# Kernel optimization log

Measured on AMD Instinct MI355X. Metric: run time of the kernel, lower is better.

Reference implementation:

```python
import jax, jax.numpy as jnp
import numpy as np

N_NODES = 50000
N_EDGES = 800000
IN_DIM = 128
OUT_DIM = 64
NEG_SLOPE = 0.2
EPS = 1e-8


def setup_inputs() -> dict:
    key = jax.random.key(0)
    k1, k2, k3, k4, k5 = jax.random.split(key, 5)
    x = jax.random.normal(k1, (N_NODES, IN_DIM), dtype=jnp.float32)
    edge_index = jax.random.randint(k2, (2, N_EDGES), 0, N_NODES, dtype=jnp.int64)
    # xavier-like scale for the linear weight
    W = jax.random.normal(k3, (IN_DIM, OUT_DIM), dtype=jnp.float32) * (1.0 / np.sqrt(IN_DIM))
    att_src = jax.random.normal(k4, (OUT_DIM,), dtype=jnp.float32) * 0.1
    att_dst = jax.random.normal(k5, (OUT_DIM,), dtype=jnp.float32) * 0.1
    bias = jnp.zeros((OUT_DIM,), dtype=jnp.float32)
    return {"x": x, "edge_index": edge_index, "W": W,
            "att_src": att_src, "att_dst": att_dst, "bias": bias}


def reference(x, edge_index, W, att_src, att_dst, bias):
    src, dst = edge_index[0], edge_index[1]
    h = x @ W                                  # (N, F_out)
    h_src = h[src]                             # (E, F_out) gather
    # per-edge score: a_src^T h_i + a_dst^T h_j
    e = h_src @ att_src + h[dst] @ att_dst     # (E,)
    e = jax.nn.leaky_relu(e, NEG_SLOPE)
    alpha = jax.nn.sigmoid(e)
    # per-dst normalization (sigmoid attention, not softmax)
    denom = jax.ops.segment_sum(alpha, dst, num_segments=N_NODES) + EPS  # (N,)
    alpha = alpha / denom[dst]
    msg = h_src * alpha[:, None]               # (E, F_out)
    out = jax.ops.segment_sum(msg, dst, num_segments=N_NODES)  # (N, F_out)
    return out + bias
```

## Files before the change

kernel.cpp:

```cpp
#include <hip/hip_runtime.h>

static constexpr int NN   = 50000;
static constexpr int NE   = 800000;
static constexpr int FIN  = 128;
static constexpr int FOUT = 64;
static constexpr int GEMM_NBLK = (NN + 63) / 64;
static constexpr int CAP  = 64;
static constexpr int NRANGE = 8;
static constexpr int RSZ  = NN / NRANGE;
static constexpr int AGG_NBLK = 2048;

static constexpr int NRG    = 196;
static constexpr int CAPSEG = 5120;
static constexpr int PA_NBLK = 98;
static constexpr int FUSE_NBLK = GEMM_NBLK + NRG;

static __device__ __forceinline__ unsigned short f2bf(float f) {
    unsigned u = __float_as_uint(f);
    u += 0x7FFFu + ((u >> 16) & 1u);
    return (unsigned short)(u >> 16);
}
static __device__ __forceinline__ float bf2f(unsigned short b) {
    return __uint_as_float(((unsigned)b) << 16);
}

__global__ __launch_bounds__(1024) void k_binA(
    const int* __restrict__ src, const int* __restrict__ dst,
    int* __restrict__ rangeCursor, unsigned int* __restrict__ epack)
{
    __shared__ int hist[NRG];
    __shared__ int base[NRG];
    const int t = threadIdx.x;
    for (int i = t; i < NRG; i += 1024) hist[i] = 0;
    __syncthreads();

    const int g = blockIdx.x * 1024 + t;
    const bool act = g < NE / 8;
    int dd[8], ss[8], rk[8], bn[8];
    if (act) {
        const int4 d0 = ((const int4*)dst)[g * 2];
        const int4 d1 = ((const int4*)dst)[g * 2 + 1];
        const int4 s0 = ((const int4*)src)[g * 2];
        const int4 s1 = ((const int4*)src)[g * 2 + 1];
        dd[0]=d0.x; dd[1]=d0.y; dd[2]=d0.z; dd[3]=d0.w;
        dd[4]=d1.x; dd[5]=d1.y; dd[6]=d1.z; dd[7]=d1.w;
        ss[0]=s0.x; ss[1]=s0.y; ss[2]=s0.z; ss[3]=s0.w;
        ss[4]=s1.x; ss[5]=s1.y; ss[6]=s1.z; ss[7]=s1.w;
        #pragma unroll
        for (int u = 0; u < 8; ++u) {
            bn[u] = dd[u] >> 8;
            rk[u] = atomicAdd(&hist[bn[u]], 1);
        }
    }
    __syncthreads();
    for (int i = t; i < NRG; i += 1024)
        base[i] = hist[i] ? atomicAdd(&rangeCursor[i], hist[i]) : 0;
    __syncthreads();
    if (act) {
        #pragma unroll
        for (int u = 0; u < 8; ++u) {
            const int pos = base[bn[u]] + rk[u];
            if (pos < CAPSEG)
                epack[bn[u] * CAPSEG + pos] =
                    ((unsigned)dd[u] << 16) | (unsigned)ss[u];
        }
    }
}

__global__ __launch_bounds__(256) void k_gemm_binB(
    const float* __restrict__ x, const float* __restrict__ W,
    const float* __restrict__ att_src, const float* __restrict__ att_dst,
    unsigned short* __restrict__ hb, float* __restrict__ ssrc,
    float* __restrict__ sdst, const int* __restrict__ rangeCursor,
    const unsigned int* __restrict__ epack, int* __restrict__ counts,
    unsigned short* __restrict__ bkt)
{
    __shared__ float4 SMEM[FIN * (FOUT / 4)];
    const int t = threadIdx.x;

    if (blockIdx.x >= GEMM_NBLK) {
        const int r = blockIdx.x - GEMM_NBLK;
        int* cur = (int*)SMEM;
        cur[t] = 0;
        __syncthreads();
        int nE = rangeCursor[r];
        if (nE > CAPSEG) nE = CAPSEG;
        for (int i = t; i < nE; i += 256) {
            const unsigned p = epack[r * CAPSEG + i];
            const int d16 = (int)(p >> 16);
            const int pos = atomicAdd(&cur[d16 & 255], 1);
            if (pos < CAP)
                bkt[(d16 << 6) + pos] = (unsigned short)(p & 0xFFFFu);
        }
        __syncthreads();
        const int node = (r << 8) + t;
        if (node < NN) counts[node] = cur[t];
        return;
    }

    float4* Ws = SMEM;
    const float4* W4 = (const float4*)W;
    #pragma unroll
    for (int i = 0; i < 8; ++i)
        Ws[t + i * 256] = W4[t + i * 256];
    __syncthreads();

    const int wave = t >> 6;
    const int lane = t & 63;
    const int rq   = lane >> 4;
    const int cq   = lane & 15;
    const int c4   = cq << 2;
    const int r0   = blockIdx.x * 64 + wave * 16 + rq * 4;

    size_t xoff[4];
    #pragma unroll
    for (int j = 0; j < 4; ++j) {
        int r = r0 + j; if (r >= NN) r = NN - 1;
        xoff[j] = (size_t)r * FIN;
    }

    float4 a0 = make_float4(0,0,0,0), a1 = a0, a2 = a0, a3 = a0;

    #pragma unroll 4
    for (int k = 0; k < FIN; k += 4) {
        const float4 xv0 = *(const float4*)(x + xoff[0] + k);
        const float4 xv1 = *(const float4*)(x + xoff[1] + k);
        const float4 xv2 = *(const float4*)(x + xoff[2] + k);
        const float4 xv3 = *(const float4*)(x + xoff[3] + k);
        const float4 w0 = Ws[(k+0) * 16 + cq];
        const float4 w1 = Ws[(k+1) * 16 + cq];
        const float4 w2 = Ws[(k+2) * 16 + cq];
        const float4 w3 = Ws[(k+3) * 16 + cq];
        a0.x += xv0.x*w0.x + xv0.y*w1.x + xv0.z*w2.x + xv0.w*w3.x;
        a0.y += xv0.x*w0.y + xv0.y*w1.y + xv0.z*w2.y + xv0.w*w3.y;
        a0.z += xv0.x*w0.z + xv0.y*w1.z + xv0.z*w2.z + xv0.w*w3.z;
        a0.w += xv0.x*w0.w + xv0.y*w1.w + xv0.z*w2.w + xv0.w*w3.w;
        a1.x += xv1.x*w0.x + xv1.y*w1.x + xv1.z*w2.x + xv1.w*w3.x;
        a1.y += xv1.x*w0.y + xv1.y*w1.y + xv1.z*w2.y + xv1.w*w3.y;
        a1.z += xv1.x*w0.z + xv1.y*w1.z + xv1.z*w2.z + xv1.w*w3.z;
        a1.w += xv1.x*w0.w + xv1.y*w1.w + xv1.z*w2.w + xv1.w*w3.w;
        a2.x += xv2.x*w0.x + xv2.y*w1.x + xv2.z*w2.x + xv2.w*w3.x;
        a2.y += xv2.x*w0.y + xv2.y*w1.y + xv2.z*w2.y + xv2.w*w3.y;
        a2.z += xv2.x*w0.z + xv2.y*w1.z + xv2.z*w2.z + xv2.w*w3.z;
        a2.w += xv2.x*w0.w + xv2.y*w1.w + xv2.z*w2.w + xv2.w*w3.w;
        a3.x += xv3.x*w0.x + xv3.y*w1.x + xv3.z*w2.x + xv3.w*w3.x;
        a3.y += xv3.x*w0.y + xv3.y*w1.y + xv3.z*w2.y + xv3.w*w3.y;
        a3.z += xv3.x*w0.z + xv3.y*w1.z + xv3.z*w2.z + xv3.w*w3.z;
        a3.w += xv3.x*w0.w + xv3.y*w1.w + xv3.z*w2.w + xv3.w*w3.w;
    }

    float4 accs[4] = {a0, a1, a2, a3};
    #pragma unroll
    for (int j = 0; j < 4; ++j) {
        if (r0 + j < NN) {
            ushort4 hv;
            hv.x = f2bf(accs[j].x); hv.y = f2bf(accs[j].y);
            hv.z = f2bf(accs[j].z); hv.w = f2bf(accs[j].w);
            *(ushort4*)(hb + (size_t)(r0 + j) * FOUT + c4) = hv;
        }
    }

    const float4 as = *(const float4*)(att_src + c4);
    const float4 ad = *(const float4*)(att_dst + c4);
    #pragma unroll
    for (int j = 0; j < 4; ++j) {
        float ps = accs[j].x*as.x + accs[j].y*as.y + accs[j].z*as.z + accs[j].w*as.w;
        float pd = accs[j].x*ad.x + accs[j].y*ad.y + accs[j].z*ad.z + accs[j].w*ad.w;
        #pragma unroll
        for (int m = 8; m >= 1; m >>= 1) {
            ps += __shfl_xor(ps, m, 64);
            pd += __shfl_xor(pd, m, 64);
        }
        if (cq == 0 && r0 + j < NN) { ssrc[r0 + j] = ps; sdst[r0 + j] = pd; }
    }
}

__global__ __launch_bounds__(256) void k_agg(
    const unsigned short* __restrict__ hb, const unsigned short* __restrict__ bkt,
    const int* __restrict__ counts, const float* __restrict__ ssrc,
    const float* __restrict__ sdst, const float* __restrict__ bias,
    float* __restrict__ out)
{
    const int r    = blockIdx.x & 7;
    const int wave = threadIdx.x >> 6;
    const int lane = threadIdx.x & 63;
    const int eq   = lane >> 3;
    const int c8   = lane & 7;
    const int c16  = c8 << 3;
    const int wstride = (AGG_NBLK >> 3) * 4;
    const float4 bLo = *(const float4*)(bias + c16);
    const float4 bHi = *(const float4*)(bias + c16 + 4);

    for (int local = (blockIdx.x >> 3) * 4 + wave; local < RSZ;
         local += 2 * wstride) {
        const int localB = local + wstride;
        const bool hasB  = localB < RSZ;
        const int nA   = r * RSZ + local;
        const int nB   = hasB ? r * RSZ + localB : nA;
        const int offA = nA << 6;
        const int offB = nB << 6;
        int cntA = counts[nA]; if (cntA > CAP) cntA = CAP;
        int cntB = hasB ? counts[nB] : 0; if (cntB > CAP) cntB = CAP;
        const float zdA = sdst[nA];
        const float zdB = sdst[nB];

        float accA[8] = {0,0,0,0,0,0,0,0};
        float accB[8] = {0,0,0,0,0,0,0,0};
        float asumA = 0.f, asumB = 0.f;

        const int nchA = (cntA + 15) >> 4;
        const int nchB = (cntB + 15) >> 4;
        const int nch  = nchA > nchB ? nchA : nchB;

        for (int c = 0; c < nch; ++c) {
            const int s0 = (c << 4) + (eq << 1);
            const unsigned wA = *(const unsigned*)(bkt + offA + s0);
            const unsigned wB = *(const unsigned*)(bkt + offB + s0);
            unsigned a0 = wA & 0xFFFFu, a1 = wA >> 16;
            unsigned b0 = wB & 0xFFFFu, b1 = wB >> 16;
            if (s0     >= cntA) a0 = 0u;
            if (s0 + 1 >= cntA) a1 = 0u;
            if (s0     >= cntB) b0 = 0u;
            if (s0 + 1 >= cntB) b1 = 0u;

            const float zA0 = ssrc[a0], zA1 = ssrc[a1];
            const float zB0 = ssrc[b0], zB1 = ssrc[b1];
            const uint4 hA0 = *(const uint4*)(hb + (size_t)a0 * FOUT + c16);
            const uint4 hA1 = *(const uint4*)(hb + (size_t)a1 * FOUT + c16);
            const uint4 hB0 = *(const uint4*)(hb + (size_t)b0 * FOUT + c16);
            const uint4 hB1 = *(const uint4*)(hb + (size_t)b1 * FOUT + c16);

            float sA0 = zA0 + zdA; sA0 = fmaxf(sA0, 0.2f * sA0);
            float sA1 = zA1 + zdA; sA1 = fmaxf(sA1, 0.2f * sA1);
            float sB0 = zB0 + zdB; sB0 = fmaxf(sB0, 0.2f * sB0);
            float sB1 = zB1 + zdB; sB1 = fmaxf(sB1, 0.2f * sB1);
            const float aA0 = (s0     < cntA) ? 1.f/(1.f+__expf(-sA0)) : 0.f;
            const float aA1 = (s0 + 1 < cntA) ? 1.f/(1.f+__expf(-sA1)) : 0.f;
            const float aB0 = (s0     < cntB) ? 1.f/(1.f+__expf(-sB0)) : 0.f;
            const float aB1 = (s0 + 1 < cntB) ? 1.f/(1.f+__expf(-sB1)) : 0.f;

            const unsigned uA0[4] = {hA0.x, hA0.y, hA0.z, hA0.w};
            const unsigned uA1[4] = {hA1.x, hA1.y, hA1.z, hA1.w};
            const unsigned uB0[4] = {hB0.x, hB0.y, hB0.z, hB0.w};
            const unsigned uB1[4] = {hB1.x, hB1.y, hB1.z, hB1.w};
            #pragma unroll
            for (int k = 0; k < 4; ++k) {
                accA[2*k]   += aA0 * bf2f((unsigned short)(uA0[k] & 0xFFFFu))
                             + aA1 * bf2f((unsigned short)(uA1[k] & 0xFFFFu));
                accA[2*k+1] += aA0 * bf2f((unsigned short)(uA0[k] >> 16))
                             + aA1 * bf2f((unsigned short)(uA1[k] >> 16));
                accB[2*k]   += aB0 * bf2f((unsigned short)(uB0[k] & 0xFFFFu))
                             + aB1 * bf2f((unsigned short)(uB1[k] & 0xFFFFu));
                accB[2*k+1] += aB0 * bf2f((unsigned short)(uB0[k] >> 16))
                             + aB1 * bf2f((unsigned short)(uB1[k] >> 16));
            }
            asumA += aA0 + aA1;
            asumB += aB0 + aB1;
        }

        #pragma unroll
        for (int m = 8; m <= 32; m <<= 1) {
            #pragma unroll
            for (int k = 0; k < 8; ++k) {
                accA[k] += __shfl_xor(accA[k], m, 64);
                accB[k] += __shfl_xor(accB[k], m, 64);
            }
            asumA += __shfl_xor(asumA, m, 64);
            asumB += __shfl_xor(asumB, m, 64);
        }

        if (eq == 0) {
            const float invA = 1.f / (asumA + 1e-8f);
            float4 lo, hi;
            lo.x = accA[0]*invA + bLo.x; lo.y = accA[1]*invA + bLo.y;
            lo.z = accA[2]*invA + bLo.z; lo.w = accA[3]*invA + bLo.w;
            hi.x = accA[4]*invA + bHi.x; hi.y = accA[5]*invA + bHi.y;
            hi.z = accA[6]*invA + bHi.z; hi.w = accA[7]*invA + bHi.w;
            *(float4*)(out + (size_t)nA * FOUT + c16)     = lo;
            *(float4*)(out + (size_t)nA * FOUT + c16 + 4) = hi;
            if (hasB) {
                const float invB = 1.f / (asumB + 1e-8f);
                lo.x = accB[0]*invB + bLo.x; lo.y = accB[1]*invB + bLo.y;
                lo.z = accB[2]*invB + bLo.z; lo.w = accB[3]*invB + bLo.w;
                hi.x = accB[4]*invB + bHi.x; hi.y = accB[5]*invB + bHi.y;
                hi.z = accB[6]*invB + bHi.z; hi.w = accB[7]*invB + bHi.w;
                *(float4*)(out + (size_t)nB * FOUT + c16)     = lo;
                *(float4*)(out + (size_t)nB * FOUT + c16 + 4) = hi;
            }
        }
    }
}

extern "C" void kernel_launch(void* const* d_in, const int* in_sizes, int n_in,
                              void* d_out, int out_size, void* d_ws, size_t ws_size,
                              hipStream_t stream)
{
    const float* x       = (const float*)d_in[0];
    const int*   ei      = (const int*)  d_in[1];
    const float* W       = (const float*)d_in[2];
    const float* att_src = (const float*)d_in[3];
    const float* att_dst = (const float*)d_in[4];
    const float* bias    = (const float*)d_in[5];
    float* out = (float*)d_out;

    unsigned short* hb  = (unsigned short*)d_ws;
    float* ssrc         = (float*)(hb + (size_t)NN * FOUT);
    float* sdst         = ssrc + NN;
    int*   counts       = (int*)(sdst + NN);
    unsigned short* bkt = (unsigned short*)(counts + NN);
    unsigned int* epack = (unsigned int*)(bkt + (size_t)NN * CAP);
    int* rangeCursor    = (int*)(epack + (size_t)NRG * CAPSEG);

    const int* src = ei;
    const int* dst = ei + NE;

    (void)hipMemsetAsync(rangeCursor, 0, NRG * sizeof(int), stream);

    k_binA<<<PA_NBLK, 1024, 0, stream>>>(src, dst, rangeCursor, epack);
    k_gemm_binB<<<FUSE_NBLK, 256, 0, stream>>>(x, W, att_src, att_dst,
                                               hb, ssrc, sdst,
                                               rangeCursor, epack,
                                               counts, bkt);
    k_agg<<<AGG_NBLK, 256, 0, stream>>>(hb, bkt, counts, ssrc, sdst,
                                        bias, out);
}
```

Measured before the change: 136.3 us.

## Compute node projection GEMM with bf16 MFMA instead of scalar FP32 FMAs

```diff
diff --git a/kernel.cpp b/kernel.cpp
--- a/kernel.cpp
+++ b/kernel.cpp
@@ -14,6 +14,11 @@
 static constexpr int CAPSEG = 5120;
 static constexpr int PA_NBLK = 98;
 static constexpr int FUSE_NBLK = GEMM_NBLK + NRG;
+
+static constexpr int WT_LD = 136;
+
+typedef short bf16x8 __attribute__((ext_vector_type(8)));
+typedef float f32x4  __attribute__((ext_vector_type(4)));
 
 static __device__ __forceinline__ unsigned short f2bf(float f) {
     unsigned u = __float_as_uint(f);
@@ -75,12 +80,12 @@
     const unsigned int* __restrict__ epack, int* __restrict__ counts,
     unsigned short* __restrict__ bkt)
 {
-    __shared__ float4 SMEM[FIN * (FOUT / 4)];
+    __shared__ alignas(16) unsigned short SML[64 * WT_LD + 4 * 1024];
     const int t = threadIdx.x;
 
     if (blockIdx.x >= GEMM_NBLK) {
         const int r = blockIdx.x - GEMM_NBLK;
-        int* cur = (int*)SMEM;
+        int* cur = (int*)SML;
         cur[t] = 0;
         __syncthreads();
         int nE = rangeCursor[r];
@@ -98,80 +103,88 @@
         return;
     }
 
-    float4* Ws = SMEM;
     const float4* W4 = (const float4*)W;
+    for (int i = t; i < 2048; i += 256) {
+        const float4 w4 = W4[i];
+        const int k = i >> 4, n0 = (i & 15) << 2;
+        SML[(n0+0) * WT_LD + k] = f2bf(w4.x);
+        SML[(n0+1) * WT_LD + k] = f2bf(w4.y);
+        SML[(n0+2) * WT_LD + k] = f2bf(w4.z);
+        SML[(n0+3) * WT_LD + k] = f2bf(w4.w);
+    }
+    __syncthreads();
+
+    const int wave  = t >> 6;
+    const int lane  = t & 63;
+    const int row16 = lane & 15;
+    const int kblk  = lane >> 4;
+    const int rbase = blockIdx.x * 64 + wave * 16;
+
+    int rowA = rbase + row16; if (rowA >= NN) rowA = NN - 1;
+    const float* xrow = x + (size_t)rowA * FIN;
+
+    f32x4 acc0 = {0,0,0,0}, acc1 = {0,0,0,0}, acc2 = {0,0,0,0}, acc3 = {0,0,0,0};
+
     #pragma unroll
-    for (int i = 0; i < 8; ++i)
-        Ws[t + i * 256] = W4[t + i * 256];
-    __syncthreads();
-
-    const int wave = t >> 6;
-    const int lane = t & 63;
-    const int rq   = lane >> 4;
-    const int cq   = lane & 15;
-    const int c4   = cq << 2;
-    const int r0   = blockIdx.x * 64 + wave * 16 + rq * 4;
-
-    size_t xoff[4];
+    for (int ks = 0; ks < 4; ++ks) {
+        const int k0 = ks * 32 + kblk * 8;
+        const float4 xa = *(const float4*)(xrow + k0);
+        const float4 xb = *(const float4*)(xrow + k0 + 4);
+        bf16x8 af;
+        af[0] = (short)f2bf(xa.x); af[1] = (short)f2bf(xa.y);
+        af[2] = (short)f2bf(xa.z); af[3] = (short)f2bf(xa.w);
+        af[4] = (short)f2bf(xb.x); af[5] = (short)f2bf(xb.y);
+        af[6] = (short)f2bf(xb.z); af[7] = (short)f2bf(xb.w);
+
+        const bf16x8 b0 = *(const bf16x8*)(&SML[(0*16 + row16) * WT_LD + k0]);
+        const bf16x8 b1 = *(const bf16x8*)(&SML[(1*16 + row16) * WT_LD + k0]);
+        const bf16x8 b2 = *(const bf16x8*)(&SML[(2*16 + row16) * WT_LD + k0]);
+        const bf16x8 b3 = *(const bf16x8*)(&SML[(3*16 + row16) * WT_LD + k0]);
+        acc0 = __builtin_amdgcn_mfma_f32_16x16x32_bf16(af, b0, acc0, 0, 0, 0);
+        acc1 = __builtin_amdgcn_mfma_f32_16x16x32_bf16(af, b1, acc1, 0, 0, 0);
+        acc2 = __builtin_amdgcn_mfma_f32_16x16x32_bf16(af, b2, acc2, 0, 0, 0);
+        acc3 = __builtin_amdgcn_mfma_f32_16x16x32_bf16(af, b3, acc3, 0, 0, 0);
+    }
+
+    float as0 = att_src[ 0 + row16], as1 = att_src[16 + row16];
+    float as2 = att_src[32 + row16], as3 = att_src[48 + row16];
+    float ad0 = att_dst[ 0 + row16], ad1 = att_dst[16 + row16];
+    float ad2 = att_dst[32 + row16], ad3 = att_dst[48 + row16];
     #pragma unroll
-    for (int j = 0; j < 4; ++j) {
-        int r = r0 + j; if (r >= NN) r = NN - 1;
-        xoff[j] = (size_t)r * FIN;
-    }
-
-    float4 a0 = make_float4(0,0,0,0), a1 = a0, a2 = a0, a3 = a0;
-
-    #pragma unroll 4
-    for (int k = 0; k < FIN; k += 4) {
-        const float4 xv0 = *(const float4*)(x + xoff[0] + k);
-        const float4 xv1 = *(const float4*)(x + xoff[1] + k);
-        const float4 xv2 = *(const float4*)(x + xoff[2] + k);
-        const float4 xv3 = *(const float4*)(x + xoff[3] + k);
-        const float4 w0 = Ws[(k+0) * 16 + cq];
-        const float4 w1 = Ws[(k+1) * 16 + cq];
-        const float4 w2 = Ws[(k+2) * 16 + cq];
-        const float4 w3 = Ws[(k+3) * 16 + cq];
-        a0.x += xv0.x*w0.x + xv0.y*w1.x + xv0.z*w2.x + xv0.w*w3.x;
-        a0.y += xv0.x*w0.y + xv0.y*w1.y + xv0.z*w2.y + xv0.w*w3.y;
-        a0.z += xv0.x*w0.z + xv0.y*w1.z + xv0.z*w2.z + xv0.w*w3.z;
-        a0.w += xv0.x*w0.w + xv0.y*w1.w + xv0.z*w2.w + xv0.w*w3.w;
-        a1.x += xv1.x*w0.x + xv1.y*w1.x + xv1.z*w2.x + xv1.w*w3.x;
-        a1.y += xv1.x*w0.y + xv1.y*w1.y + xv1.z*w2.y + xv1.w*w3.y;
-        a1.z += xv1.x*w0.z + xv1.y*w1.z + xv1.z*w2.z + xv1.w*w3.z;
-        a1.w += xv1.x*w0.w + xv1.y*w1.w + xv1.z*w2.w + xv1.w*w3.w;
-        a2.x += xv2.x*w0.x + xv2.y*w1.x + xv2.z*w2.x + xv2.w*w3.x;
-        a2.y += xv2.x*w0.y + xv2.y*w1.y + xv2.z*w2.y + xv2.w*w3.y;
-        a2.z += xv2.x*w0.z + xv2.y*w1.z + xv2.z*w2.z + xv2.w*w3.z;
-        a2.w += xv2.x*w0.w + xv2.y*w1.w + xv2.z*w2.w + xv2.w*w3.w;
-        a3.x += xv3.x*w0.x + xv3.y*w1.x + xv3.z*w2.x + xv3.w*w3.x;
-        a3.y += xv3.x*w0.y + xv3.y*w1.y + xv3.z*w2.y + xv3.w*w3.y;
-        a3.z += xv3.x*w0.z + xv3.y*w1.z + xv3.z*w2.z + xv3.w*w3.z;
-        a3.w += xv3.x*w0.w + xv3.y*w1.w + xv3.z*w2.w + xv3.w*w3.w;
-    }
-
-    float4 accs[4] = {a0, a1, a2, a3};
+    for (int reg = 0; reg < 4; ++reg) {
+        float p = acc0[reg]*as0 + acc1[reg]*as1 + acc2[reg]*as2 + acc3[reg]*as3;
+        float q = acc0[reg]*ad0 + acc1[reg]*ad1 + acc2[reg]*ad2 + acc3[reg]*ad3;
+        #pragma unroll
+        for (int m = 1; m <= 8; m <<= 1) {
+            p += __shfl_xor(p, m, 64);
+            q += __shfl_xor(q, m, 64);
+        }
+        if (row16 == 0) {
+            const int r = rbase + kblk * 4 + reg;
+            if (r < NN) { ssrc[r] = p; sdst[r] = q; }
+        }
+    }
+
+    unsigned short* hT = SML + 64 * WT_LD + wave * 1024;
     #pragma unroll
-    for (int j = 0; j < 4; ++j) {
-        if (r0 + j < NN) {
-            ushort4 hv;
-            hv.x = f2bf(accs[j].x); hv.y = f2bf(accs[j].y);
-            hv.z = f2bf(accs[j].z); hv.w = f2bf(accs[j].w);
-            *(ushort4*)(hb + (size_t)(r0 + j) * FOUT + c4) = hv;
-        }
-    }
-
-    const float4 as = *(const float4*)(att_src + c4);
-    const float4 ad = *(const float4*)(att_dst + c4);
-    #pragma unroll
-    for (int j = 0; j < 4; ++j) {
-        float ps = accs[j].x*as.x + accs[j].y*as.y + accs[j].z*as.z + accs[j].w*as.w;
-        float pd = accs[j].x*ad.x + accs[j].y*ad.y + accs[j].z*ad.z + accs[j].w*ad.w;
-        #pragma unroll
-        for (int m = 8; m >= 1; m >>= 1) {
-            ps += __shfl_xor(ps, m, 64);
-            pd += __shfl_xor(pd, m, 64);
-        }
-        if (cq == 0 && r0 + j < NN) { ssrc[r0 + j] = ps; sdst[r0 + j] = pd; }
+    for (int reg = 0; reg < 4; ++reg) {
+        const int rr = (kblk * 4 + reg) * 64;
+        hT[rr +  0 + row16] = f2bf(acc0[reg]);
+        hT[rr + 16 + row16] = f2bf(acc1[reg]);
+        hT[rr + 32 + row16] = f2bf(acc2[reg]);
+        hT[rr + 48 + row16] = f2bf(acc3[reg]);
+    }
+    __syncthreads();
+    {
+        const int rr = lane >> 2;
+        const int cc = (lane & 3) << 4;
+        const int grow = rbase + rr;
+        if (grow < NN) {
+            const uint4 v0 = *(const uint4*)(hT + rr * 64 + cc);
+            const uint4 v1 = *(const uint4*)(hT + rr * 64 + cc + 8);
+            *(uint4*)(hb + (size_t)grow * FOUT + cc)     = v0;
+            *(uint4*)(hb + (size_t)grow * FOUT + cc + 8) = v1;
+        }
     }
 }
 
```

Measured after the change: 128.9 us, median of 2. 1.06x faster.
